# Kernel optimization log

Hardware: AMD Instinct MI355X
Metric: run time of the kernel (lower is better)

The kernel has to match this reference:

```python
import jax, jax.numpy as jnp
import numpy as np

N_NODES = 100000
N_EDGES = 1600000
IN_CH, HID, OUT_CH = 500, 128, 40


def setup_inputs() -> dict:
    key = jax.random.key(0)
    ks = jax.random.split(key, 10)
    x = jax.random.normal(ks[0], (N_NODES, IN_CH), dtype=jnp.float32)
    edge_index = jax.random.randint(ks[1], (2, N_EDGES), 0, N_NODES, dtype=jnp.int64)
    edge_attr = jax.random.uniform(ks[2], (N_EDGES,), dtype=jnp.float32)
    def glorot(k, fan_in, fan_out):
        s = jnp.sqrt(6.0 / (fan_in + fan_out))
        return jax.random.uniform(k, (fan_in, fan_out), minval=-s, maxval=s, dtype=jnp.float32)
    return {
        "x": x, "edge_index": edge_index, "edge_attr": edge_attr,
        "W1": glorot(ks[3], IN_CH, HID), "b1": jnp.zeros((HID,), jnp.float32),
        "W2": glorot(ks[4], HID, HID), "b2": jnp.zeros((HID,), jnp.float32),
        "W3": glorot(ks[5], HID, OUT_CH), "b3": jnp.zeros((OUT_CH,), jnp.float32),
    }


def _gcn_norm(edge_index, edge_weight, num_nodes):
    # add self-loops with weight 1, then symmetric normalization D^-1/2 A D^-1/2
    loop = jnp.arange(num_nodes, dtype=edge_index.dtype)
    src = jnp.concatenate([edge_index[0], loop])
    dst = jnp.concatenate([edge_index[1], loop])
    ew = jnp.concatenate([edge_weight, jnp.ones((num_nodes,), edge_weight.dtype)])
    deg = jax.ops.segment_sum(ew, dst, num_segments=num_nodes)
    dinv = jnp.where(deg > 0, jax.lax.rsqrt(jnp.maximum(deg, 1e-12)), 0.0)
    norm = dinv[src] * ew * dinv[dst]
    return src, dst, norm


def _gcn_conv(x, W, b, src, dst, norm, num_nodes):
    h = x @ W                                   # [N, F_out] dense transform first
    msg = h[src] * norm[:, None]                # gather + scale  [E+N, F_out]
    out = jax.ops.segment_sum(msg, dst, num_segments=num_nodes)
    return out + b


def reference(x, edge_index, edge_attr, W1, b1, W2, b2, W3, b3):
    n = x.shape[0]
    src, dst, norm = _gcn_norm(edge_index, edge_attr, n)  # cached=False but graph is static
    # layer 1 (hidden) + relu + residual-dense (h_res starts at 0); dropout is identity in eval
    h = jax.nn.relu(_gcn_conv(x, W1, b1, src, dst, norm, n))
    h_res = h
    # layer 2 (hidden)
    h = jax.nn.relu(_gcn_conv(h, W2, b2, src, dst, norm, n)) + h_res
    # output layer
    out = _gcn_conv(h, W3, b3, src, dst, norm, n)
    return jax.nn.log_softmax(out, axis=-1)
```

## Files before the change

### kernel.cpp

```cpp
#include <hip/hip_runtime.h>
#include <hip/hip_bf16.h>
#include <type_traits>

#define NN 100000
#define NE 1600000

#define SCAN_E 1024
#define NBLK ((NN + SCAN_E - 1) / SCAN_E)
#define GBLK ((NN + 127) / 128)
#define EBLK ((NE + 511) / 512)

using f32x4 = __attribute__((ext_vector_type(4))) float;
using bf16x8 = __attribute__((ext_vector_type(8))) short;
using u16 = unsigned short;
using u64 = unsigned long long;

__device__ inline u16 f2bf(float f) {
    unsigned u = __float_as_uint(f);
    unsigned r = (u + 0x7fffu + ((u >> 16) & 1u)) >> 16;
    return (u16)r;
}
__device__ inline float bflo(unsigned u) { return __uint_as_float(u << 16); }
__device__ inline float bfhi(unsigned u) { return __uint_as_float(u & 0xffff0000u); }
__device__ inline float bf2f(u16 u) { return __uint_as_float((unsigned)u << 16); }
__device__ inline unsigned cvt2(float a, float b) {
    union { __hip_bfloat162 h; unsigned u; } c;
    c.h = __float22bfloat162_rn(make_float2(a, b));
    return c.u;
}

template <typename AT, int KLIM, int KSTEPS, bool TAIL>
__device__ __forceinline__ void gemm_body(const AT* __restrict__ X,
                                          const short* __restrict__ Wp,
                                          u16* __restrict__ Out) {
    const int lane = threadIdx.x & 63;
    const int wave = threadIdx.x >> 6;
    const int row0 = blockIdx.x * 128 + wave * 16;
    const int arow = row0 + (lane & 15);
    const int kgrp = (lane >> 4) << 3;
    const bool rvalid = arow < NN;
    const AT* aptr = X + (size_t)arow * KLIM + kgrp;
    const bf16x8* wp = reinterpret_cast<const bf16x8*>(Wp);

    f32x4 acc[8];
#pragma unroll
    for (int nt = 0; nt < 8; nt++) acc[nt] = (f32x4){0.f, 0.f, 0.f, 0.f};

    const int FULL = TAIL ? (KSTEPS - 1) : KSTEPS;
#pragma unroll 2
    for (int ks = 0; ks < FULL; ks++) {
        bf16x8 af;
        if (rvalid) {
            if constexpr (std::is_same_v<AT, float>) {
                float4 f0 = *reinterpret_cast<const float4*>(aptr + ks * 32);
                float4 f1 = *reinterpret_cast<const float4*>(aptr + ks * 32 + 4);
                union { bf16x8 v; unsigned u[4]; } a;
                a.u[0] = cvt2(f0.x, f0.y);
                a.u[1] = cvt2(f0.z, f0.w);
                a.u[2] = cvt2(f1.x, f1.y);
                a.u[3] = cvt2(f1.z, f1.w);
                af = a.v;
            } else {
                af = *reinterpret_cast<const bf16x8*>(aptr + ks * 32);
            }
        } else {
#pragma unroll
            for (int j = 0; j < 8; j++) af[j] = 0;
        }
#pragma unroll
        for (int nt = 0; nt < 8; nt++) {
            bf16x8 bf = wp[(ks * 8 + nt) * 64 + lane];
            acc[nt] = __builtin_amdgcn_mfma_f32_16x16x32_bf16(af, bf, acc[nt], 0, 0, 0);
        }
    }
    if (TAIL) {
        const int ks = KSTEPS - 1;
        bf16x8 af;
#pragma unroll
        for (int j = 0; j < 8; j++) {
            int k = ks * 32 + kgrp + j;
            bool ok = rvalid && k < KLIM;
            if constexpr (std::is_same_v<AT, float>) {
                af[j] = (short)f2bf(ok ? aptr[ks * 32 + j] : 0.f);
            } else {
                af[j] = ok ? (short)aptr[ks * 32 + j] : (short)0;
            }
        }
#pragma unroll
        for (int nt = 0; nt < 8; nt++) {
            bf16x8 bf = wp[(ks * 8 + nt) * 64 + lane];
            acc[nt] = __builtin_amdgcn_mfma_f32_16x16x32_bf16(af, bf, acc[nt], 0, 0, 0);
        }
    }

    const int rbase = row0 + ((lane >> 4) << 2);
    const int cbase = lane & 15;
#pragma unroll
    for (int r = 0; r < 4; r++) {
        int orow = rbase + r;
        if (orow < NN) {
            u16* p = Out + (size_t)orow * 128 + cbase;
#pragma unroll
            for (int nt = 0; nt < 8; nt += 2) {
                unsigned v = cvt2(acc[nt][r], acc[nt + 1][r]);
                p[nt * 16] = (u16)v;
                p[nt * 16 + 16] = (u16)(v >> 16);
            }
        }
    }
}

__global__ __launch_bounds__(512) void k_gemm1_deg(const float* __restrict__ X,
                                                   const short* __restrict__ Wp,
                                                   u16* __restrict__ Out,
                                                   const int* __restrict__ ei,
                                                   const float* __restrict__ ea,
                                                   u64* __restrict__ dc,
                                                   int* __restrict__ rank) {
    if (blockIdx.x >= GBLK) {
        int e = (blockIdx.x - GBLK) * 512 + threadIdx.x;
        if (e < NE) {
            int d = ei[NE + e];
            u64 add = (1ULL << 32) | (u64)(unsigned)(ea[e] * 16777216.0f);
            u64 old = atomicAdd(dc + d, add);
            rank[e] = (int)(old >> 32);
        }
        return;
    }
    gemm_body<float, 500, 16, true>(X, Wp, Out);
}

template <typename AT, int KLIM, int KSTEPS, bool TAIL>
__global__ __launch_bounds__(512) void k_gemm_mfma(const AT* __restrict__ X,
                                                   const short* __restrict__ Wp,
                                                   u16* __restrict__ Out) {
    gemm_body<AT, KLIM, KSTEPS, TAIL>(X, Wp, Out);
}

__global__ __launch_bounds__(256) void k_dinv(const u64* __restrict__ dc,
                                              float* __restrict__ dinv) {
    int i = blockIdx.x * 256 + threadIdx.x;
    if (i < NN) {
        uint2 v = reinterpret_cast<const uint2*>(dc)[i];
        float d = (float)v.x * (1.0f / 16777216.0f) + 1.0f;
        dinv[i] = rsqrtf(d);
    }
}

__global__ __launch_bounds__(256) void k_scan1(const u64* __restrict__ dc,
                                               int* __restrict__ row_ptr,
                                               int* __restrict__ part) {
    __shared__ int ts[256];
    const int tid = threadIdx.x;
    int base = blockIdx.x * SCAN_E + tid * 4;
    int v[4];
    int ssum = 0;
#pragma unroll
    for (int j = 0; j < 4; j++) {
        v[j] = (base + j < NN) ? (int)(dc[base + j] >> 32) : 0;
        ssum += v[j];
    }
    ts[tid] = ssum;
    __syncthreads();
    for (int o = 1; o < 256; o <<= 1) {
        int t = (tid >= o) ? ts[tid - o] : 0;
        __syncthreads();
        ts[tid] += t;
        __syncthreads();
    }
    int excl = ts[tid] - ssum;
#pragma unroll
    for (int j = 0; j < 4; j++) {
        if (base + j < NN) row_ptr[base + j] = excl;
        excl += v[j];
    }
    if (tid == 255) part[blockIdx.x] = ts[255];
}

__global__ void k_scan2(int* __restrict__ part) {
    if (threadIdx.x == 0) {
        int acc = 0;
        for (int b = 0; b < NBLK; b++) { int t = part[b]; part[b] = acc; acc += t; }
    }
}

__global__ __launch_bounds__(256) void k_scan3(int* __restrict__ row_ptr,
                                               const int* __restrict__ part) {
    int base = blockIdx.x * SCAN_E + threadIdx.x * 4;
    int off = part[blockIdx.x];
#pragma unroll
    for (int j = 0; j < 4; j++)
        if (base + j < NN) row_ptr[base + j] += off;
    if (blockIdx.x == 0 && threadIdx.x == 0) row_ptr[NN] = NE;
}

__global__ __launch_bounds__(256) void k_scatter(const int* __restrict__ ei,
                                                 const float* __restrict__ ea,
                                                 const float* __restrict__ dinv,
                                                 const int* __restrict__ row_ptr,
                                                 const int* __restrict__ rank,
                                                 int2* __restrict__ csr) {
    int e = blockIdx.x * 256 + threadIdx.x;
    if (e >= NE) return;
    int s = ei[e], d = ei[NE + e];
    int pos = row_ptr[d] + rank[e];
    float w = dinv[s] * ea[e] * dinv[d];
    csr[pos] = make_int2(s, __float_as_int(w));
}

__global__ __launch_bounds__(256) void k_packW(const float* __restrict__ W,
                                               short* __restrict__ Wp,
                                               int K, int total) {
    int t = blockIdx.x * 256 + threadIdx.x;
    if (t >= total) return;
    int lane = t & 63;
    int nt = (t >> 6) & 7;
    int ks = t >> 9;
    int col = nt * 16 + (lane & 15);
    int kb = ks * 32 + ((lane >> 4) << 3);
    bf16x8 v;
#pragma unroll
    for (int j = 0; j < 8; j++) {
        int k = kb + j;
        v[j] = (k < K) ? (short)f2bf(W[(size_t)k * 128 + col]) : (short)0;
    }
    reinterpret_cast<bf16x8*>(Wp)[t] = v;
}

__global__ __launch_bounds__(256) void k_gemm40(const u16* __restrict__ Xb,
                                                const float* __restrict__ W,
                                                u16* __restrict__ Out) {
    __shared__ float xs[128][32];
    const int tid = threadIdx.x;
    const int col = tid & 63;
    const int rbase = (tid >> 6) * 8;
    const int row0 = blockIdx.x * 32;

    for (int idx = tid; idx < 1024; idx += 256) {
        int r = idx & 31;
        int k4 = idx >> 5;
        uint2 v = *reinterpret_cast<const uint2*>(Xb + (size_t)(row0 + r) * 128 + k4 * 4);
        xs[k4 * 4 + 0][r] = bflo(v.x);
        xs[k4 * 4 + 1][r] = bfhi(v.x);
        xs[k4 * 4 + 2][r] = bflo(v.y);
        xs[k4 * 4 + 3][r] = bfhi(v.y);
    }
    __syncthreads();

    float acc[8];
#pragma unroll
    for (int i = 0; i < 8; i++) acc[i] = 0.f;

#pragma unroll 2
    for (int k = 0; k < 128; k++) {
        float w = (col < 40) ? W[k * 40 + col] : 0.f;
        const float* xr = &xs[k][rbase];
#pragma unroll
        for (int i = 0; i < 8; i++) acc[i] = fmaf(xr[i], w, acc[i]);
    }
    if (col < 40) {
#pragma unroll
        for (int i = 0; i < 8; i++)
            Out[(size_t)(row0 + rbase + i) * 40 + col] = f2bf(acc[i]);
    }
}

template <int MODE>
__global__ __launch_bounds__(256) void k_pull128(const u16* __restrict__ H,
                                                 const int* __restrict__ row_ptr,
                                                 const int2* __restrict__ csr,
                                                 const float* __restrict__ dinv,
                                                 const float* __restrict__ b,
                                                 const u16* __restrict__ R,
                                                 u16* __restrict__ Out) {
    int node = blockIdx.x * 8 + (threadIdx.x >> 5);
    int cg = threadIdx.x & 31;
    const uint2* H2 = reinterpret_cast<const uint2*>(H);
    float dv = dinv[node];
    float sw = dv * dv;
    uint2 h = H2[node * 32 + cg];
    float4 acc;
    acc.x = bflo(h.x) * sw; acc.y = bfhi(h.x) * sw;
    acc.z = bflo(h.y) * sw; acc.w = bfhi(h.y) * sw;

    int e0 = row_ptr[node], e1 = row_ptr[node + 1];
    for (int base = e0; base < e1; base += 32) {
        int n = e1 - base;
        if (n > 32) n = 32;
        int2 sv = (cg < n) ? csr[base + cg] : make_int2(0, 0);
        int j = 0;
        for (; j + 4 <= n; j += 4) {
            int s0 = __shfl(sv.x, j + 0, 32);
            int s1 = __shfl(sv.x, j + 1, 32);
            int s2 = __shfl(sv.x, j + 2, 32);
            int s3 = __shfl(sv.x, j + 3, 32);
            float w0 = __int_as_float(__shfl(sv.y, j + 0, 32));
            float w1 = __int_as_float(__shfl(sv.y, j + 1, 32));
            float w2 = __int_as_float(__shfl(sv.y, j + 2, 32));
            float w3 = __int_as_float(__shfl(sv.y, j + 3, 32));
            uint2 g0 = H2[s0 * 32 + cg];
            uint2 g1 = H2[s1 * 32 + cg];
            uint2 g2 = H2[s2 * 32 + cg];
            uint2 g3 = H2[s3 * 32 + cg];
            acc.x = fmaf(w0, bflo(g0.x), acc.x); acc.y = fmaf(w0, bfhi(g0.x), acc.y);
            acc.z = fmaf(w0, bflo(g0.y), acc.z); acc.w = fmaf(w0, bfhi(g0.y), acc.w);
            acc.x = fmaf(w1, bflo(g1.x), acc.x); acc.y = fmaf(w1, bfhi(g1.x), acc.y);
            acc.z = fmaf(w1, bflo(g1.y), acc.z); acc.w = fmaf(w1, bfhi(g1.y), acc.w);
            acc.x = fmaf(w2, bflo(g2.x), acc.x); acc.y = fmaf(w2, bfhi(g2.x), acc.y);
            acc.z = fmaf(w2, bflo(g2.y), acc.z); acc.w = fmaf(w2, bfhi(g2.y), acc.w);
            acc.x = fmaf(w3, bflo(g3.x), acc.x); acc.y = fmaf(w3, bfhi(g3.x), acc.y);
            acc.z = fmaf(w3, bflo(g3.y), acc.z); acc.w = fmaf(w3, bfhi(g3.y), acc.w);
        }
        for (; j < n; j++) {
            int s = __shfl(sv.x, j, 32);
            float w = __int_as_float(__shfl(sv.y, j, 32));
            uint2 g = H2[s * 32 + cg];
            acc.x = fmaf(w, bflo(g.x), acc.x); acc.y = fmaf(w, bfhi(g.x), acc.y);
            acc.z = fmaf(w, bflo(g.y), acc.z); acc.w = fmaf(w, bfhi(g.y), acc.w);
        }
    }

    float4 bb = reinterpret_cast<const float4*>(b)[cg];
    float4 o;
    o.x = fmaxf(acc.x + bb.x, 0.f);
    o.y = fmaxf(acc.y + bb.y, 0.f);
    o.z = fmaxf(acc.z + bb.z, 0.f);
    o.w = fmaxf(acc.w + bb.w, 0.f);
    if (MODE == 2) {
        uint2 r = reinterpret_cast<const uint2*>(R)[node * 32 + cg];
        o.x += bflo(r.x); o.y += bfhi(r.x);
        o.z += bflo(r.y); o.w += bfhi(r.y);
    }
    reinterpret_cast<uint2*>(Out)[node * 32 + cg] =
        make_uint2(cvt2(o.x, o.y), cvt2(o.z, o.w));
}

__global__ __launch_bounds__(256) void k_pull40_lsm(const u16* __restrict__ G,
                                                    const int* __restrict__ row_ptr,
                                                    const int2* __restrict__ csr,
                                                    const float* __restrict__ dinv,
                                                    const float* __restrict__ b3,
                                                    float* __restrict__ out) {
    int node = blockIdx.x * 4 + (threadIdx.x >> 6);
    int lane = threadIdx.x & 63;
    const bool act = lane < 40;
    float dv = dinv[node];
    float sw = dv * dv;
    float acc = act ? bf2f(G[node * 40 + lane]) * sw : 0.f;

    int e0 = row_ptr[node], e1 = row_ptr[node + 1];
    for (int base = e0; base < e1; base += 64) {
        int n = e1 - base;
        if (n > 64) n = 64;
        int2 sv = (lane < n) ? csr[base + lane] : make_int2(0, 0);
        int j = 0;
        for (; j + 4 <= n; j += 4) {
            int s0 = __shfl(sv.x, j + 0);
            int s1 = __shfl(sv.x, j + 1);
            int s2 = __shfl(sv.x, j + 2);
            int s3 = __shfl(sv.x, j + 3);
            float w0 = __int_as_float(__shfl(sv.y, j + 0));
            float w1 = __int_as_float(__shfl(sv.y, j + 1));
            float w2 = __int_as_float(__shfl(sv.y, j + 2));
            float w3 = __int_as_float(__shfl(sv.y, j + 3));
            float g0 = act ? bf2f(G[s0 * 40 + lane]) : 0.f;
            float g1 = act ? bf2f(G[s1 * 40 + lane]) : 0.f;
            float g2 = act ? bf2f(G[s2 * 40 + lane]) : 0.f;
            float g3 = act ? bf2f(G[s3 * 40 + lane]) : 0.f;
            acc = fmaf(w0, g0, acc);
            acc = fmaf(w1, g1, acc);
            acc = fmaf(w2, g2, acc);
            acc = fmaf(w3, g3, acc);
        }
        for (; j < n; j++) {
            int s = __shfl(sv.x, j);
            float w = __int_as_float(__shfl(sv.y, j));
            float g = act ? bf2f(G[s * 40 + lane]) : 0.f;
            acc = fmaf(w, g, acc);
        }
    }

    float v = act ? acc + b3[lane] : -1e30f;
    float m = v;
    for (int o = 32; o; o >>= 1) m = fmaxf(m, __shfl_xor(m, o));
    float e = act ? expf(v - m) : 0.f;
    float ssum = e;
    for (int o = 32; o; o >>= 1) ssum += __shfl_xor(ssum, o);
    float ls = logf(ssum);
    if (act) out[node * 40 + lane] = v - m - ls;
}

extern "C" void kernel_launch(void* const* d_in, const int* in_sizes, int n_in,
                              void* d_out, int out_size, void* d_ws, size_t ws_size,
                              hipStream_t stream) {
    const float* x  = (const float*)d_in[0];
    const int*   ei = (const int*)d_in[1];
    const float* ea = (const float*)d_in[2];
    const float* W1 = (const float*)d_in[3];
    const float* b1 = (const float*)d_in[4];
    const float* W2 = (const float*)d_in[5];
    const float* b2 = (const float*)d_in[6];
    const float* W3 = (const float*)d_in[7];
    const float* b3 = (const float*)d_in[8];
    float* out = (float*)d_out;

    short* Wp1     = (short*)d_ws;
    short* Wp2     = Wp1 + 65536;
    u16*   Hb      = (u16*)(Wp2 + 16384);
    u16*   h1b     = Hb + (size_t)NN * 128;
    u16*   G3b     = h1b + (size_t)NN * 128;
    u64*   dc      = (u64*)(G3b + (size_t)NN * 40);
    float* dinv    = (float*)(dc + NN);
    int*   row_ptr = (int*)(dinv + NN);
    int*   part    = row_ptr + NN + 8;
    int*   rank    = part + 128;
    int2*  csr     = (int2*)(rank + NE);

    hipMemsetAsync(dc, 0, NN * sizeof(u64), stream);
    k_packW<<<32, 256, 0, stream>>>(W1, Wp1, 500, 16 * 8 * 64);
    k_packW<<<8, 256, 0, stream>>>(W2, Wp2, 128, 4 * 8 * 64);

    k_gemm1_deg<<<GBLK + EBLK, 512, 0, stream>>>(x, Wp1, Hb, ei, ea, dc, rank);

    k_dinv<<<(NN + 255) / 256, 256, 0, stream>>>(dc, dinv);
    k_scan1<<<NBLK, 256, 0, stream>>>(dc, row_ptr, part);
    k_scan2<<<1, 64, 0, stream>>>(part);
    k_scan3<<<NBLK, 256, 0, stream>>>(row_ptr, part);
    k_scatter<<<(NE + 255) / 256, 256, 0, stream>>>(ei, ea, dinv, row_ptr, rank, csr);

    k_pull128<1><<<NN / 8, 256, 0, stream>>>(Hb, row_ptr, csr, dinv, b1, nullptr, h1b);

    k_gemm_mfma<u16, 128, 4, false><<<GBLK, 512, 0, stream>>>(h1b, Wp2, Hb);
    k_pull128<2><<<NN / 8, 256, 0, stream>>>(Hb, row_ptr, csr, dinv, b2, h1b, h1b);

    k_gemm40<<<NN / 32, 256, 0, stream>>>(h1b, W3, G3b);
    k_pull40_lsm<<<NN / 4, 256, 0, stream>>>(G3b, row_ptr, csr, dinv, b3, out);
}
```

Before: 514.5 us.

## Split layer-1 GEMM across degree and scatter kernels, MFMA for output GEMM

The layer-1 GEMM is split into two halves. One half is co-launched with the degree-counting atomics and the other with the CSR scatter, so the small edge kernels overlap with dense compute. The dinv computation is folded into the first scan kernel, which removes one launch. The scalar FP32 128x40 output GEMM is replaced by a bf16 MFMA kernel with a prepacked, zero-padded W3. This cuts launches and idle gaps between dependent stages, at the cost of placing the edge and GEMM blocks in the same grid, where they compete for resources.

After: 526.2 us. 2.3% more time.

```diff
diff --git a/kernel.cpp b/kernel.cpp
--- a/kernel.cpp
+++ b/kernel.cpp
@@ -9,6 +9,8 @@
 #define NBLK ((NN + SCAN_E - 1) / SCAN_E)
 #define GBLK ((NN + 127) / 128)
 #define EBLK ((NE + 511) / 512)
+#define GA1 512
+#define GB1 (GBLK - GA1)
 
 using f32x4 = __attribute__((ext_vector_type(4))) float;
 using bf16x8 = __attribute__((ext_vector_type(8))) short;
@@ -32,10 +34,10 @@
 template <typename AT, int KLIM, int KSTEPS, bool TAIL>
 __device__ __forceinline__ void gemm_body(const AT* __restrict__ X,
                                           const short* __restrict__ Wp,
-                                          u16* __restrict__ Out) {
+                                          u16* __restrict__ Out, int gblk) {
     const int lane = threadIdx.x & 63;
     const int wave = threadIdx.x >> 6;
-    const int row0 = blockIdx.x * 128 + wave * 16;
+    const int row0 = gblk * 128 + wave * 16;
     const int arow = row0 + (lane & 15);
     const int kgrp = (lane >> 4) << 3;
     const bool rvalid = arow < NN;
@@ -110,15 +112,15 @@
     }
 }
 
-__global__ __launch_bounds__(512) void k_gemm1_deg(const float* __restrict__ X,
-                                                   const short* __restrict__ Wp,
-                                                   u16* __restrict__ Out,
-                                                   const int* __restrict__ ei,
-                                                   const float* __restrict__ ea,
-                                                   u64* __restrict__ dc,
-                                                   int* __restrict__ rank) {
-    if (blockIdx.x >= GBLK) {
-        int e = (blockIdx.x - GBLK) * 512 + threadIdx.x;
+__global__ __launch_bounds__(512) void k_deg_gemm1a(const float* __restrict__ X,
+                                                    const short* __restrict__ Wp,
+                                                    u16* __restrict__ Out,
+                                                    const int* __restrict__ ei,
+                                                    const float* __restrict__ ea,
+                                                    u64* __restrict__ dc,
+                                                    int* __restrict__ rank) {
+    if (blockIdx.x < EBLK) {
+        int e = blockIdx.x * 512 + threadIdx.x;
         if (e < NE) {
             int d = ei[NE + e];
             u64 add = (1ULL << 32) | (u64)(unsigned)(ea[e] * 16777216.0f);
@@ -127,29 +129,42 @@
         }
         return;
     }
-    gemm_body<float, 500, 16, true>(X, Wp, Out);
+    gemm_body<float, 500, 16, true>(X, Wp, Out, blockIdx.x - EBLK);
+}
+
+__global__ __launch_bounds__(512) void k_scat_gemm1b(const float* __restrict__ X,
+                                                     const short* __restrict__ Wp,
+                                                     u16* __restrict__ Out,
+                                                     const int* __restrict__ ei,
+                                                     const float* __restrict__ ea,
+                                                     const float* __restrict__ dinv,
+                                                     const int* __restrict__ row_ptr,
+                                                     const int* __restrict__ rank,
+                                                     int2* __restrict__ csr) {
+    if (blockIdx.x < EBLK) {
+        int e = blockIdx.x * 512 + threadIdx.x;
+        if (e < NE) {
+            int s = ei[e], d = ei[NE + e];
+            int pos = row_ptr[d] + rank[e];
+            float w = dinv[s] * ea[e] * dinv[d];
+            csr[pos] = make_int2(s, __float_as_int(w));
+        }
+        return;
+    }
+    gemm_body<float, 500, 16, true>(X, Wp, Out, blockIdx.x - EBLK + GA1);
 }
 
 template <typename AT, int KLIM, int KSTEPS, bool TAIL>
 __global__ __launch_bounds__(512) void k_gemm_mfma(const AT* __restrict__ X,
                                                    const short* __restrict__ Wp,
                                                    u16* __restrict__ Out) {
-    gemm_body<AT, KLIM, KSTEPS, TAIL>(X, Wp, Out);
-}
-
-__global__ __launch_bounds__(256) void k_dinv(const u64* __restrict__ dc,
-                                              float* __restrict__ dinv) {
-    int i = blockIdx.x * 256 + threadIdx.x;
-    if (i < NN) {
-        uint2 v = reinterpret_cast<const uint2*>(dc)[i];
-        float d = (float)v.x * (1.0f / 16777216.0f) + 1.0f;
-        dinv[i] = rsqrtf(d);
-    }
+    gemm_body<AT, KLIM, KSTEPS, TAIL>(X, Wp, Out, blockIdx.x);
 }
 
 __global__ __launch_bounds__(256) void k_scan1(const u64* __restrict__ dc,
                                                int* __restrict__ row_ptr,
-                                               int* __restrict__ part) {
+                                               int* __restrict__ part,
+                                               float* __restrict__ dinv) {
     __shared__ int ts[256];
     const int tid = threadIdx.x;
     int base = blockIdx.x * SCAN_E + tid * 4;
@@ -157,7 +172,13 @@
     int ssum = 0;
 #pragma unroll
     for (int j = 0; j < 4; j++) {
-        v[j] = (base + j < NN) ? (int)(dc[base + j] >> 32) : 0;
+        if (base + j < NN) {
+            uint2 d2 = reinterpret_cast<const uint2*>(dc)[base + j];
+            v[j] = (int)d2.y;
+            dinv[base + j] = rsqrtf((float)d2.x * (1.0f / 16777216.0f) + 1.0f);
+        } else {
+            v[j] = 0;
+        }
         ssum += v[j];
     }
     ts[tid] = ssum;
@@ -192,20 +213,6 @@
     for (int j = 0; j < 4; j++)
         if (base + j < NN) row_ptr[base + j] += off;
     if (blockIdx.x == 0 && threadIdx.x == 0) row_ptr[NN] = NE;
-}
-
-__global__ __launch_bounds__(256) void k_scatter(const int* __restrict__ ei,
-                                                 const float* __restrict__ ea,
-                                                 const float* __restrict__ dinv,
-                                                 const int* __restrict__ row_ptr,
-                                                 const int* __restrict__ rank,
-                                                 int2* __restrict__ csr) {
-    int e = blockIdx.x * 256 + threadIdx.x;
-    if (e >= NE) return;
-    int s = ei[e], d = ei[NE + e];
-    int pos = row_ptr[d] + rank[e];
-    float w = dinv[s] * ea[e] * dinv[d];
-    csr[pos] = make_int2(s, __float_as_int(w));
 }
 
 __global__ __launch_bounds__(256) void k_packW(const float* __restrict__ W,
@@ -227,41 +234,65 @@
     reinterpret_cast<bf16x8*>(Wp)[t] = v;
 }
 
-__global__ __launch_bounds__(256) void k_gemm40(const u16* __restrict__ Xb,
-                                                const float* __restrict__ W,
-                                                u16* __restrict__ Out) {
-    __shared__ float xs[128][32];
-    const int tid = threadIdx.x;
-    const int col = tid & 63;
-    const int rbase = (tid >> 6) * 8;
-    const int row0 = blockIdx.x * 32;
-
-    for (int idx = tid; idx < 1024; idx += 256) {
-        int r = idx & 31;
-        int k4 = idx >> 5;
-        uint2 v = *reinterpret_cast<const uint2*>(Xb + (size_t)(row0 + r) * 128 + k4 * 4);
-        xs[k4 * 4 + 0][r] = bflo(v.x);
-        xs[k4 * 4 + 1][r] = bfhi(v.x);
-        xs[k4 * 4 + 2][r] = bflo(v.y);
-        xs[k4 * 4 + 3][r] = bfhi(v.y);
-    }
-    __syncthreads();
-
-    float acc[8];
-#pragma unroll
-    for (int i = 0; i < 8; i++) acc[i] = 0.f;
-
-#pragma unroll 2
-    for (int k = 0; k < 128; k++) {
-        float w = (col < 40) ? W[k * 40 + col] : 0.f;
-        const float* xr = &xs[k][rbase];
-#pragma unroll
-        for (int i = 0; i < 8; i++) acc[i] = fmaf(xr[i], w, acc[i]);
-    }
-    if (col < 40) {
-#pragma unroll
-        for (int i = 0; i < 8; i++)
-            Out[(size_t)(row0 + rbase + i) * 40 + col] = f2bf(acc[i]);
+__global__ __launch_bounds__(256) void k_packW3(const float* __restrict__ W,
+                                                short* __restrict__ Wp) {
+    int t = blockIdx.x * 256 + threadIdx.x;
+    if (t >= 768) return;
+    int lane = t & 63;
+    int nt = (t >> 6) % 3;
+    int ks = t / 192;
+    int col = nt * 16 + (lane & 15);
+    int kb = ks * 32 + ((lane >> 4) << 3);
+    bf16x8 v;
+#pragma unroll
+    for (int j = 0; j < 8; j++)
+        v[j] = (col < 40) ? (short)f2bf(W[(size_t)(kb + j) * 40 + col]) : (short)0;
+    reinterpret_cast<bf16x8*>(Wp)[t] = v;
+}
+
+__global__ __launch_bounds__(512) void k_gemm40m(const u16* __restrict__ Xb,
+                                                 const short* __restrict__ Wp,
+                                                 u16* __restrict__ Out) {
+    const int lane = threadIdx.x & 63;
+    const int wave = threadIdx.x >> 6;
+    const int row0 = blockIdx.x * 128 + wave * 16;
+    const int arow = row0 + (lane & 15);
+    const int kgrp = (lane >> 4) << 3;
+    const bool rvalid = arow < NN;
+    const u16* aptr = Xb + (size_t)arow * 128 + kgrp;
+    const bf16x8* wp = reinterpret_cast<const bf16x8*>(Wp);
+
+    f32x4 acc[3];
+#pragma unroll
+    for (int nt = 0; nt < 3; nt++) acc[nt] = (f32x4){0.f, 0.f, 0.f, 0.f};
+
+#pragma unroll
+    for (int ks = 0; ks < 4; ks++) {
+        bf16x8 af;
+        if (rvalid) af = *reinterpret_cast<const bf16x8*>(aptr + ks * 32);
+        else {
+#pragma unroll
+            for (int j = 0; j < 8; j++) af[j] = 0;
+        }
+#pragma unroll
+        for (int nt = 0; nt < 3; nt++) {
+            bf16x8 bf = wp[(ks * 3 + nt) * 64 + lane];
+            acc[nt] = __builtin_amdgcn_mfma_f32_16x16x32_bf16(af, bf, acc[nt], 0, 0, 0);
+        }
+    }
+
+    const int rbase = row0 + ((lane >> 4) << 2);
+    const int cbase = lane & 15;
+#pragma unroll
+    for (int r = 0; r < 4; r++) {
+        int orow = rbase + r;
+        if (orow < NN) {
+#pragma unroll
+            for (int nt = 0; nt < 3; nt++) {
+                int col = nt * 16 + cbase;
+                if (col < 40) Out[(size_t)orow * 40 + col] = f2bf(acc[nt][r]);
+            }
+        }
     }
 }
 
@@ -406,7 +437,8 @@
 
     short* Wp1     = (short*)d_ws;
     short* Wp2     = Wp1 + 65536;
-    u16*   Hb      = (u16*)(Wp2 + 16384);
+    short* Wp3     = Wp2 + 16384;
+    u16*   Hb      = (u16*)(Wp3 + 6144);
     u16*   h1b     = Hb + (size_t)NN * 128;
     u16*   G3b     = h1b + (size_t)NN * 128;
     u64*   dc      = (u64*)(G3b + (size_t)NN * 40);
@@ -419,20 +451,22 @@
     hipMemsetAsync(dc, 0, NN * sizeof(u64), stream);
     k_packW<<<32, 256, 0, stream>>>(W1, Wp1, 500, 16 * 8 * 64);
     k_packW<<<8, 256, 0, stream>>>(W2, Wp2, 128, 4 * 8 * 64);
-
-    k_gemm1_deg<<<GBLK + EBLK, 512, 0, stream>>>(x, Wp1, Hb, ei, ea, dc, rank);
-
-    k_dinv<<<(NN + 255) / 256, 256, 0, stream>>>(dc, dinv);
-    k_scan1<<<NBLK, 256, 0, stream>>>(dc, row_ptr, part);
+    k_packW3<<<3, 256, 0, stream>>>(W3, Wp3);
+
+    k_deg_gemm1a<<<EBLK + GA1, 512, 0, stream>>>(x, Wp1, Hb, ei, ea, dc, rank);
+
+    k_scan1<<<NBLK, 256, 0, stream>>>(dc, row_ptr, part, dinv);
     k_scan2<<<1, 64, 0, stream>>>(part);
     k_scan3<<<NBLK, 256, 0, stream>>>(row_ptr, part);
-    k_scatter<<<(NE + 255) / 256, 256, 0, stream>>>(ei, ea, dinv, row_ptr, rank, csr);
+
+    k_scat_gemm1b<<<EBLK + GB1, 512, 0, stream>>>(x, Wp1, Hb, ei, ea, dinv,
+                                                  row_ptr, rank, csr);
 
     k_pull128<1><<<NN / 8, 256, 0, stream>>>(Hb, row_ptr, csr, dinv, b1, nullptr, h1b);
 
     k_gemm_mfma<u16, 128, 4, false><<<GBLK, 512, 0, stream>>>(h1b, Wp2, Hb);
     k_pull128<2><<<NN / 8, 256, 0, stream>>>(Hb, row_ptr, csr, dinv, b2, h1b, h1b);
 
-    k_gemm40<<<NN / 32, 256, 0, stream>>>(h1b, W3, G3b);
+    k_gemm40m<<<GBLK, 512, 0, stream>>>(h1b, Wp3, G3b);
     k_pull40_lsm<<<NN / 4, 256, 0, stream>>>(G3b, row_ptr, csr, dinv, b3, out);
 }
```
